# Optimization experiments

Hardware: AMD Instinct MI355X
Metric: run time of the kernel (lower is better)

The kernel has to match this reference:

```python
import jax, jax.numpy as jnp
import numpy as np

N = 8192
IN_F = 300
OUT_F = 300
ALPHA = 0.3  # leaky relu slope
NEG_INF = -1e12


def setup_inputs() -> dict:
    key = jax.random.key(0)
    k1, k2, k3, k4, k5 = jax.random.split(key, 5)
    inp = jax.random.normal(k1, (N, IN_F), dtype=jnp.float32)
    adj = jax.random.randint(k2, (N, N), 0, 2, dtype=jnp.int32)
    # xavier-uniform-like init for params
    def xavier(k, shape):
        fan_in, fan_out = shape[0], shape[1]
        limit = 1.414 * (6.0 / (fan_in + fan_out)) ** 0.5
        return jax.random.uniform(k, shape, jnp.float32, -limit, limit)
    W = xavier(k3, (IN_F, OUT_F))
    a = xavier(k4, (2 * OUT_F, 1))
    wtrans = xavier(k5, (2 * IN_F, OUT_F))
    return {"inp": inp, "adj": adj, "W": W, "a": a, "wtrans": wtrans}


def reference(inp, adj, W, a, wtrans):
    # h: [N, OUT_F]
    h = inp @ W
    Wh1 = h @ a[:OUT_F, :]          # [N, 1]
    Wh2 = h @ a[OUT_F:, :]          # [N, 1]
    e = jax.nn.leaky_relu(Wh1 + Wh2.T, negative_slope=ALPHA)  # [N, N]
    mask = adj > 0
    attention = jax.nn.softmax(jnp.where(mask, e, NEG_INF), axis=1)
    negative_attention = -jax.nn.softmax(jnp.where(mask, -e, NEG_INF), axis=1)
    # dropout p=0.0 / eval mode -> identity
    h_prime = attention @ inp                 # [N, IN_F]
    h_prime_negative = negative_attention @ inp
    h_prime_double = jnp.concatenate([h_prime, h_prime_negative], axis=1)  # [N, 2*IN_F]
    new_h_prime = h_prime_double @ wtrans     # [N, OUT_F]
    return jax.nn.elu(new_h_prime)  # concat=True
```

## Files before the change

kernel.cpp:

```cpp
#include <hip/hip_runtime.h>
#include <stdint.h>

#define NROW 8192
#define LOG2E 1.4426950408889634f
#define ALPHA 0.3f

#define WA1_OFF 0
#define WA2_OFF 512
#define S1_OFF 1024
#define S2_OFF (1024 + 8192)
#define SCAL_OFF (S2_OFF + 8192)
#define PQB_OFF 70656
#define PQB_BYTES (256 * 40960)
#define PART_OFF (PQB_OFF + PQB_BYTES)

typedef _Float16 f16x8 __attribute__((ext_vector_type(8)));
typedef __fp16 fp16x2 __attribute__((ext_vector_type(2)));
typedef float f32x4 __attribute__((ext_vector_type(4)));

union HPack { fp16x2 h2[4]; f16x8 v; uint32_t u[4]; };
union HBits { _Float16 h[2]; uint32_t u; };

__device__ __forceinline__ int swz(int col, int g) { return (g + (col >> 1)) & 3; }

__global__ void k_wa(const float* __restrict__ Wm, const float* __restrict__ a,
                     float* __restrict__ wsf) {
  int r = blockIdx.x * 4 + (threadIdx.x >> 6);
  int ln = threadIdx.x & 63;
  if (r >= 300) return;
  float a1 = 0.f, a2 = 0.f;
  for (int c = ln; c < 300; c += 64) {
    float w = Wm[r * 300 + c];
    a1 += w * a[c];
    a2 += w * a[300 + c];
  }
  for (int o = 32; o; o >>= 1) { a1 += __shfl_down(a1, o); a2 += __shfl_down(a2, o); }
  if (!ln) { wsf[WA1_OFF + r] = a1; wsf[WA2_OFF + r] = a2; }
}

__global__ void k_s12(const float* __restrict__ inp, float* __restrict__ wsf) {
  int row = blockIdx.x * 4 + (threadIdx.x >> 6);
  int ln = threadIdx.x & 63;
  const float* ip = inp + (size_t)row * 300;
  float a1 = 0.f, a2 = 0.f;
  for (int c = ln; c < 300; c += 64) {
    float v = ip[c];
    a1 += v * wsf[WA1_OFF + c];
    a2 += v * wsf[WA2_OFF + c];
  }
  for (int o = 32; o; o >>= 1) { a1 += __shfl_down(a1, o); a2 += __shfl_down(a2, o); }
  if (!ln) { wsf[S1_OFF + row] = a1 * LOG2E; wsf[S2_OFF + row] = a2 * LOG2E; }
}

__global__ void k_minmax(float* __restrict__ wsf) {
  int t = threadIdx.x;
  float mx = -3e38f, mn = 3e38f;
  for (int i = t; i < NROW; i += 1024) {
    float v = wsf[S2_OFF + i];
    mx = fmaxf(mx, v); mn = fminf(mn, v);
  }
  for (int o = 32; o; o >>= 1) {
    mx = fmaxf(mx, __shfl_down(mx, o));
    mn = fminf(mn, __shfl_down(mn, o));
  }
  __shared__ float sm[32];
  int wv = t >> 6, ln = t & 63;
  if (!ln) { sm[wv] = mx; sm[16 + wv] = mn; }
  __syncthreads();
  if (!t) {
    float M = sm[0], m = sm[16];
    for (int q = 1; q < 16; q++) { M = fmaxf(M, sm[q]); m = fminf(m, sm[16 + q]); }
    wsf[SCAL_OFF] = M; wsf[SCAL_OFF + 1] = m;
  }
}

__global__ __launch_bounds__(640) void k_wt(const float* __restrict__ inp,
                                            const float* __restrict__ wt,
                                            uint16_t* __restrict__ pqb) {
  __shared__ float L[300 * 36];
  const int kb = blockIdx.x;
  const int t = threadIdx.x;
  const float* src = inp + (size_t)kb * 32 * 300;
  for (int idx = t; idx < 9600; idx += 640) {
    int j = idx / 300;
    int c = idx - j * 300;
    L[c * 36 + j] = src[idx];
  }
  __syncthreads();
  if (t < 608) {
    const int pq = (t >= 304) ? 1 : 0;
    const int f = t - pq * 304;
    float acc[32];
    if (f < 300) {
      #pragma unroll
      for (int q = 0; q < 32; q++) acc[q] = 0.f;
      const float* wcol = wt + (size_t)pq * 90000 + f;
      for (int c = 0; c < 300; c++) {
        float wv = wcol[(size_t)c * 300];
        const float4* lp = (const float4*)(L + c * 36);
        #pragma unroll
        for (int q = 0; q < 8; q++) {
          float4 v = lp[q];
          acc[q * 4 + 0] += v.x * wv;
          acc[q * 4 + 1] += v.y * wv;
          acc[q * 4 + 2] += v.z * wv;
          acc[q * 4 + 3] += v.w * wv;
        }
      }
    } else {
      float cv = (f == 300) ? 1.0f : 0.0f;
      #pragma unroll
      for (int q = 0; q < 32; q++) acc[q] = cv;
    }
    uint16_t* dst = pqb + (size_t)kb * 20480 + (size_t)pq * 10240 + (size_t)f * 32;
    #pragma unroll
    for (int g = 0; g < 4; g++) {
      const int gs = swz(f, g);
      uint32_t* d32 = (uint32_t*)(dst + gs * 8);
      #pragma unroll
      for (int i = 0; i < 4; i++) {
        HBits hb;
        hb.h[0] = (_Float16)acc[g * 8 + 2 * i];
        hb.h[1] = (_Float16)acc[g * 8 + 2 * i + 1];
        d32[i] = hb.u;
      }
    }
  }
}

__global__ __launch_bounds__(256, 2) void k_main(const int* __restrict__ adj,
                                                 const float* __restrict__ wsf,
                                                 const uint16_t* __restrict__ pqb,
                                                 float* __restrict__ part, int nsplit) {
  __shared__ __align__(16) uint16_t Bsm[2][2 * 320 * 32];
  const int bid = blockIdx.x;
  const int mblk = bid / nsplit;
  const int ks = bid - mblk * nsplit;
  const int tid = threadIdx.x;
  const int w = tid >> 6, lane = tid & 63;
  const int lr = lane & 15, lg = lane >> 4;
  const int row = mblk * 64 + w * 16 + lr;
  const float c1 = wsf[S1_OFF + row];
  const float s2mx = wsf[SCAL_OFF];
  const float s2mn = wsf[SCAL_OFF + 1];
  float t1 = c1 + s2mx; const float mxp = fmaxf(t1, ALPHA * t1);
  float t2 = c1 + s2mn; const float mn2 = fmaxf(t2, ALPHA * t2);
  const int kcnt = NROW / nsplit;
  const int k0 = ks * kcnt;
  const int ksteps = kcnt >> 5;
  const int tb0 = k0 >> 5;
  const int* adjrow = adj + (size_t)row * NROW;
  f32x4 accP[19], accN[19];
  const f32x4 zero = {0.f, 0.f, 0.f, 0.f};
  #pragma unroll
  for (int ct = 0; ct < 19; ct++) { accP[ct] = zero; accN[ct] = zero; }

  auto STAGE = [&](int b, int tb) {
    const char* tile = (const char*)(pqb + (size_t)tb * 20480);
    char* dst = (char*)Bsm[b];
    #pragma unroll
    for (int it = 0; it < 10; it++) {
      const int off = (w * 10 + it) * 1024;
      __builtin_amdgcn_global_load_lds(
          (const __attribute__((address_space(1))) void*)(tile + off + lane * 16),
          (__attribute__((address_space(3))) void*)(dst + off),
          16, 0, 0);
    }
  };

  STAGE(0, tb0);
  const int kw0 = k0 + lg * 8;
  int4 cA0 = *(const int4*)(adjrow + kw0);
  int4 cA1 = *(const int4*)(adjrow + kw0 + 4);
  float4 cS0 = *(const float4*)(wsf + S2_OFF + kw0);
  float4 cS1 = *(const float4*)(wsf + S2_OFF + kw0 + 4);
  __syncthreads();

  for (int s = 0; s < ksteps; s++) {
    const int cur = s & 1;
    const int sn = (s + 1 < ksteps) ? s + 1 : s;
    STAGE(cur ^ 1, tb0 + sn);
    const int kwn = k0 + sn * 32 + lg * 8;
    const int4 nA0 = *(const int4*)(adjrow + kwn);
    const int4 nA1 = *(const int4*)(adjrow + kwn + 4);
    const float4 nS0 = *(const float4*)(wsf + S2_OFF + kwn);
    const float4 nS1 = *(const float4*)(wsf + S2_OFF + kwn + 4);

    float se[8] = {cS0.x, cS0.y, cS0.z, cS0.w, cS1.x, cS1.y, cS1.z, cS1.w};
    int am[8] = {cA0.x, cA0.y, cA0.z, cA0.w, cA1.x, cA1.y, cA1.z, cA1.w};
    HPack up, un;
    #pragma unroll
    for (int e = 0; e < 8; e += 2) {
      float ea = c1 + se[e];     ea = fmaxf(ea, ALPHA * ea);
      float eb = c1 + se[e + 1]; eb = fmaxf(eb, ALPHA * eb);
      float pa = exp2f(ea - mxp);
      float pb = exp2f(eb - mxp);
      float na = exp2f(mn2 - ea);
      float nb = exp2f(mn2 - eb);
      pa = am[e] ? pa : 0.0f;     na = am[e] ? na : 0.0f;
      pb = am[e + 1] ? pb : 0.0f; nb = am[e + 1] ? nb : 0.0f;
      up.h2[e >> 1] = __builtin_amdgcn_cvt_pkrtz(pa, pb);
      un.h2[e >> 1] = __builtin_amdgcn_cvt_pkrtz(na, nb);
    }

    const char* smc = (const char*)Bsm[cur];
    #pragma unroll
    for (int ct = 0; ct < 19; ct++) {
      const int col = ct * 16 + lr;
      const int gp = swz(col, lg);
      f16x8 bP = *(const f16x8*)(smc + col * 64 + gp * 16);
      f16x8 bN = *(const f16x8*)(smc + 20480 + col * 64 + gp * 16);
      accP[ct] = __builtin_amdgcn_mfma_f32_16x16x32_f16(up.v, bP, accP[ct], 0, 0, 0);
      accN[ct] = __builtin_amdgcn_mfma_f32_16x16x32_f16(un.v, bN, accN[ct], 0, 0, 0);
    }

    __syncthreads();

    cA0 = nA0; cA1 = nA1; cS0 = nS0; cS1 = nS1;
  }

  const int orow = mblk * 64 + w * 16 + lg * 4;
  float* pbase = part + ((size_t)ks * NROW + orow) * 608;
  #pragma unroll
  for (int ct = 0; ct < 19; ct++) {
    const int col = ct * 16 + lr;
    #pragma unroll
    for (int r = 0; r < 4; r++) {
      pbase[(size_t)r * 608 + col] = accP[ct][r];
      pbase[(size_t)r * 608 + 304 + col] = accN[ct][r];
    }
  }
}

__global__ void k_final(const float* __restrict__ part, float* __restrict__ out, int nsplit) {
  const int i = blockIdx.x;
  const int t = threadIdx.x;
  if (t >= 300) return;
  float sp = 0.f, sn = 0.f, zp = 0.f, zn = 0.f;
  for (int s = 0; s < nsplit; s++) {
    const float* p = part + ((size_t)s * NROW + i) * 608;
    sp += p[t];
    sn += p[304 + t];
    zp += p[300];
    zn += p[604];
  }
  float x = sp / zp - sn / zn;
  out[(size_t)i * 300 + t] = (x > 0.f) ? x : (exp2f(x * LOG2E) - 1.0f);
}

extern "C" void kernel_launch(void* const* d_in, const int* in_sizes, int n_in,
                              void* d_out, int out_size, void* d_ws, size_t ws_size,
                              hipStream_t stream) {
  const float* inp = (const float*)d_in[0];
  const int* adj = (const int*)d_in[1];
  const float* Wm = (const float*)d_in[2];
  const float* a = (const float*)d_in[3];
  const float* wt = (const float*)d_in[4];
  float* out = (float*)d_out;
  float* wsf = (float*)d_ws;
  uint16_t* pqb = (uint16_t*)((char*)d_ws + PQB_OFF);
  float* part = (float*)((char*)d_ws + PART_OFF);

  int nsplit = 4;
  while (nsplit > 1 &&
         (size_t)PART_OFF + (size_t)nsplit * NROW * 608 * 4 > ws_size)
    nsplit >>= 1;

  k_wa<<<75, 256, 0, stream>>>(Wm, a, wsf);
  k_s12<<<NROW / 4, 256, 0, stream>>>(inp, wsf);
  k_minmax<<<1, 1024, 0, stream>>>(wsf);
  k_wt<<<256, 640, 0, stream>>>(inp, wt, pqb);
  k_main<<<128 * nsplit, 256, 0, stream>>>(adj, wsf, pqb, part, nsplit);
  k_final<<<NROW, 320, 0, stream>>>(part, out, nsplit);
}
```

Before: 264.9 us.

## Split waves by softmax side so each B fragment feeds two row tiles

Each wave now handles one side (positive or negative softmax) for 32 rows instead of both sides for 16 rows. One LDS B-fragment read is reused by two MFMAs, which halves LDS read traffic per MFMA. In exchange, each wave issues twice the adjacency loads (two rows per lane), and the per-lane side selection adds a few VALU selects. Total MFMA and exp counts are unchanged.

```diff
diff --git a/kernel.cpp b/kernel.cpp
--- a/kernel.cpp
+++ b/kernel.cpp
@@ -139,21 +139,26 @@
   const int tid = threadIdx.x;
   const int w = tid >> 6, lane = tid & 63;
   const int lr = lane & 15, lg = lane >> 4;
-  const int row = mblk * 64 + w * 16 + lr;
-  const float c1 = wsf[S1_OFF + row];
-  const float s2mx = wsf[SCAL_OFF];
-  const float s2mn = wsf[SCAL_OFF + 1];
-  float t1 = c1 + s2mx; const float mxp = fmaxf(t1, ALPHA * t1);
-  float t2 = c1 + s2mn; const float mn2 = fmaxf(t2, ALPHA * t2);
+  const int side = w & 1;
+  const int rg = w >> 1;
+  const int rbase = mblk * 64 + rg * 32;
+  const int row0 = rbase + lr;
+  const int row1 = rbase + 16 + lr;
+  const float c1_0 = wsf[S1_OFF + row0];
+  const float c1_1 = wsf[S1_OFF + row1];
+  const float s2ref = side ? wsf[SCAL_OFF + 1] : wsf[SCAL_OFF];
+  float tt0 = c1_0 + s2ref; const float off0 = fmaxf(tt0, ALPHA * tt0);
+  float tt1 = c1_1 + s2ref; const float off1 = fmaxf(tt1, ALPHA * tt1);
   const int kcnt = NROW / nsplit;
   const int k0 = ks * kcnt;
   const int ksteps = kcnt >> 5;
   const int tb0 = k0 >> 5;
-  const int* adjrow = adj + (size_t)row * NROW;
-  f32x4 accP[19], accN[19];
+  const int* adjr0 = adj + (size_t)row0 * NROW;
+  const int* adjr1 = adj + (size_t)row1 * NROW;
+  f32x4 acc0[19], acc1[19];
   const f32x4 zero = {0.f, 0.f, 0.f, 0.f};
   #pragma unroll
-  for (int ct = 0; ct < 19; ct++) { accP[ct] = zero; accN[ct] = zero; }
+  for (int ct = 0; ct < 19; ct++) { acc0[ct] = zero; acc1[ct] = zero; }
 
   auto STAGE = [&](int b, int tb) {
     const char* tile = (const char*)(pqb + (size_t)tb * 20480);
@@ -170,8 +175,10 @@
 
   STAGE(0, tb0);
   const int kw0 = k0 + lg * 8;
-  int4 cA0 = *(const int4*)(adjrow + kw0);
-  int4 cA1 = *(const int4*)(adjrow + kw0 + 4);
+  int4 cA00 = *(const int4*)(adjr0 + kw0);
+  int4 cA01 = *(const int4*)(adjr0 + kw0 + 4);
+  int4 cA10 = *(const int4*)(adjr1 + kw0);
+  int4 cA11 = *(const int4*)(adjr1 + kw0 + 4);
   float4 cS0 = *(const float4*)(wsf + S2_OFF + kw0);
   float4 cS1 = *(const float4*)(wsf + S2_OFF + kw0 + 4);
   __syncthreads();
@@ -181,53 +188,58 @@
     const int sn = (s + 1 < ksteps) ? s + 1 : s;
     STAGE(cur ^ 1, tb0 + sn);
     const int kwn = k0 + sn * 32 + lg * 8;
-    const int4 nA0 = *(const int4*)(adjrow + kwn);
-    const int4 nA1 = *(const int4*)(adjrow + kwn + 4);
+    const int4 nA00 = *(const int4*)(adjr0 + kwn);
+    const int4 nA01 = *(const int4*)(adjr0 + kwn + 4);
+    const int4 nA10 = *(const int4*)(adjr1 + kwn);
+    const int4 nA11 = *(const int4*)(adjr1 + kwn + 4);
     const float4 nS0 = *(const float4*)(wsf + S2_OFF + kwn);
     const float4 nS1 = *(const float4*)(wsf + S2_OFF + kwn + 4);
 
     float se[8] = {cS0.x, cS0.y, cS0.z, cS0.w, cS1.x, cS1.y, cS1.z, cS1.w};
-    int am[8] = {cA0.x, cA0.y, cA0.z, cA0.w, cA1.x, cA1.y, cA1.z, cA1.w};
-    HPack up, un;
+    int am0[8] = {cA00.x, cA00.y, cA00.z, cA00.w, cA01.x, cA01.y, cA01.z, cA01.w};
+    int am1[8] = {cA10.x, cA10.y, cA10.z, cA10.w, cA11.x, cA11.y, cA11.z, cA11.w};
+    HPack up0, up1;
     #pragma unroll
     for (int e = 0; e < 8; e += 2) {
-      float ea = c1 + se[e];     ea = fmaxf(ea, ALPHA * ea);
-      float eb = c1 + se[e + 1]; eb = fmaxf(eb, ALPHA * eb);
-      float pa = exp2f(ea - mxp);
-      float pb = exp2f(eb - mxp);
-      float na = exp2f(mn2 - ea);
-      float nb = exp2f(mn2 - eb);
-      pa = am[e] ? pa : 0.0f;     na = am[e] ? na : 0.0f;
-      pb = am[e + 1] ? pb : 0.0f; nb = am[e + 1] ? nb : 0.0f;
-      up.h2[e >> 1] = __builtin_amdgcn_cvt_pkrtz(pa, pb);
-      un.h2[e >> 1] = __builtin_amdgcn_cvt_pkrtz(na, nb);
-    }
-
-    const char* smc = (const char*)Bsm[cur];
+      float e0a = c1_0 + se[e];     e0a = fmaxf(e0a, ALPHA * e0a);
+      float e0b = c1_0 + se[e + 1]; e0b = fmaxf(e0b, ALPHA * e0b);
+      float e1a = c1_1 + se[e];     e1a = fmaxf(e1a, ALPHA * e1a);
+      float e1b = c1_1 + se[e + 1]; e1b = fmaxf(e1b, ALPHA * e1b);
+      float d0a = side ? (off0 - e0a) : (e0a - off0);
+      float d0b = side ? (off0 - e0b) : (e0b - off0);
+      float d1a = side ? (off1 - e1a) : (e1a - off1);
+      float d1b = side ? (off1 - e1b) : (e1b - off1);
+      float p0a = exp2f(d0a); p0a = am0[e] ? p0a : 0.0f;
+      float p0b = exp2f(d0b); p0b = am0[e + 1] ? p0b : 0.0f;
+      float p1a = exp2f(d1a); p1a = am1[e] ? p1a : 0.0f;
+      float p1b = exp2f(d1b); p1b = am1[e + 1] ? p1b : 0.0f;
+      up0.h2[e >> 1] = __builtin_amdgcn_cvt_pkrtz(p0a, p0b);
+      up1.h2[e >> 1] = __builtin_amdgcn_cvt_pkrtz(p1a, p1b);
+    }
+
+    const char* half = (const char*)Bsm[cur] + side * 20480;
     #pragma unroll
     for (int ct = 0; ct < 19; ct++) {
       const int col = ct * 16 + lr;
       const int gp = swz(col, lg);
-      f16x8 bP = *(const f16x8*)(smc + col * 64 + gp * 16);
-      f16x8 bN = *(const f16x8*)(smc + 20480 + col * 64 + gp * 16);
-      accP[ct] = __builtin_amdgcn_mfma_f32_16x16x32_f16(up.v, bP, accP[ct], 0, 0, 0);
-      accN[ct] = __builtin_amdgcn_mfma_f32_16x16x32_f16(un.v, bN, accN[ct], 0, 0, 0);
+      f16x8 b = *(const f16x8*)(half + col * 64 + gp * 16);
+      acc0[ct] = __builtin_amdgcn_mfma_f32_16x16x32_f16(up0.v, b, acc0[ct], 0, 0, 0);
+      acc1[ct] = __builtin_amdgcn_mfma_f32_16x16x32_f16(up1.v, b, acc1[ct], 0, 0, 0);
     }
 
     __syncthreads();
 
-    cA0 = nA0; cA1 = nA1; cS0 = nS0; cS1 = nS1;
-  }
-
-  const int orow = mblk * 64 + w * 16 + lg * 4;
-  float* pbase = part + ((size_t)ks * NROW + orow) * 608;
+    cA00 = nA00; cA01 = nA01; cA10 = nA10; cA11 = nA11; cS0 = nS0; cS1 = nS1;
+  }
+
+  float* pb = part + ((size_t)ks * NROW + rbase) * 608 + (size_t)side * 304;
   #pragma unroll
   for (int ct = 0; ct < 19; ct++) {
     const int col = ct * 16 + lr;
     #pragma unroll
     for (int r = 0; r < 4; r++) {
-      pbase[(size_t)r * 608 + col] = accP[ct][r];
-      pbase[(size_t)r * 608 + 304 + col] = accN[ct][r];
+      pb[(size_t)(lg * 4 + r) * 608 + col] = acc0[ct][r];
+      pb[(size_t)(16 + lg * 4 + r) * 608 + col] = acc1[ct][r];
     }
   }
 }
```

Measured after the change: 273.4 us. 3.2% more time.
